# Optimization experiments

Measured on AMD Instinct MI355X. Metric: run time of the kernel, lower is better.

The kernel has to match this reference:

```python
import jax, jax.numpy as jnp
import numpy as np

WS = 8          # window_size
HEADS = 8
HEAD_DIM = 32
DIM = 256       # input_dim
DISP = WS // 2  # displacement for shifted windows
SCALE = HEAD_DIM ** -0.5
NEG = float('-inf')


def _create_mask(upper_lower, left_right):
    S = WS * WS
    m = np.zeros((S, S), np.float32)
    if upper_lower:
        m[-DISP * WS:, :-DISP * WS] = NEG
        m[:-DISP * WS, -DISP * WS:] = NEG
    if left_right:
        m = m.reshape(WS, WS, WS, WS)
        m[:, -DISP:, :, :-DISP] = NEG
        m[:, :-DISP, :, -DISP:] = NEG
        m = m.reshape(S, S)
    return m


def _shift_mask(nwh, nww):
    # per-window additive mask, [nW, S, S]
    S = WS * WS
    low = _create_mask(True, False)
    right = _create_mask(False, True)
    mask = np.zeros((nwh * nww, S, S), np.float32)
    mask[-nww:] += low                 # bottom row of windows
    mask[nww - 1::nww] += right        # rightmost column of windows
    return mask


def _rel_idx():
    coords = np.array([[x, y] for x in range(WS) for y in range(WS)])
    dist = coords[None, :, :] - coords[:, None, :] + (WS - 1)  # in [0, 2*WS-2]
    return dist[..., 0], dist[..., 1]


def setup_inputs() -> dict:
    key = jax.random.key(0)
    ks = jax.random.split(key, 5)
    B, H, W = 64, 64, 64
    inner = HEADS * HEAD_DIM
    return {
        "x": jax.random.normal(ks[0], (B, H, W, DIM), jnp.float32),
        "qkv_w": jax.random.normal(ks[1], (3 * inner, DIM), jnp.float32) * 0.02,
        "proj_w": jax.random.normal(ks[2], (DIM, inner), jnp.float32) * 0.02,
        "proj_b": jnp.zeros((DIM,), jnp.float32),
        "pos_emb": jax.random.normal(ks[3], (2 * WS - 1, 2 * WS - 1), jnp.float32),
    }


def reference(x, qkv_w, proj_w, proj_b, pos_emb):
    B, H, W, C = x.shape
    nwh, nww = H // WS, W // WS
    nW, S = nwh * nww, WS * WS

    x = jnp.roll(x, (-DISP, -DISP), axis=(1, 2))          # cyclic shift
    qkv = x @ qkv_w.T                                      # [B,H,W,3*inner]
    q, k, v = jnp.split(qkv, 3, axis=-1)

    def towin(t):  # [B,H,W,heads*d] -> [B,heads,nW,S,d]
        t = t.reshape(B, nwh, WS, nww, WS, HEADS, HEAD_DIM)
        return t.transpose(0, 5, 1, 3, 2, 4, 6).reshape(B, HEADS, nW, S, HEAD_DIM)

    q, k, v = towin(q), towin(k), towin(v)

    scores = jnp.einsum('bhwid,bhwjd->bhwij', q, k) * SCALE
    ri, ci = _rel_idx()
    scores = scores + pos_emb[ri, ci]                      # relative position bias [S,S]
    mask = jnp.asarray(_shift_mask(nwh, nww))              # [nW,S,S]
    scores = scores + mask[None, None]

    attn = jax.nn.softmax(scores, axis=-1)
    out = jnp.einsum('bhwij,bhwjd->bhwid', attn, v)        # [B,heads,nW,S,d]

    out = out.reshape(B, HEADS, nwh, nww, WS, WS, HEAD_DIM)
    out = out.transpose(0, 2, 4, 3, 5, 1, 6).reshape(B, H, W, HEADS * HEAD_DIM)

    out = out @ proj_w.T + proj_b
    out = jnp.roll(out, (DISP, DISP), axis=(1, 2))         # reverse cyclic shift
    return out
```

## Files before the change

kernel.cpp:

```cpp
#include <hip/hip_runtime.h>
#include <hip/hip_bf16.h>
#include <math.h>

typedef __bf16 bf16;
typedef bf16 bf16x8 __attribute__((ext_vector_type(8)));
typedef bf16 bf16x4 __attribute__((ext_vector_type(4)));
typedef float f32x4 __attribute__((ext_vector_type(4)));

#define MFMA16(A,B,C) __builtin_amdgcn_mfma_f32_16x16x32_bf16(A,B,C,0,0,0)

static constexpr int QKV_ELEMS  = 768 * 256;
static constexpr int PROJ_ELEMS = 256 * 256;

static __device__ __forceinline__ void lds_fence() {
    asm volatile("s_waitcnt lgkmcnt(0)" ::: "memory");
    __builtin_amdgcn_sched_barrier(0);
}

__global__ void cvt_weights(const float* __restrict__ qkv_w,
                            const float* __restrict__ proj_w,
                            bf16* __restrict__ wq, bf16* __restrict__ wp) {
    int i = blockIdx.x * 256 + threadIdx.x;
    if (i < QKV_ELEMS) wq[i] = (bf16)qkv_w[i];
    int j = i - QKV_ELEMS;
    if (j >= 0 && j < PROJ_ELEMS) wp[j] = (bf16)proj_w[j];
}

__global__ __launch_bounds__(512, 2)
void swin_fused(const float* __restrict__ x,
                const bf16* __restrict__ wqkv,
                const bf16* __restrict__ wproj,
                const float* __restrict__ proj_b,
                const float* __restrict__ pose_g,
                float* __restrict__ out)
{
    __shared__ alignas(16) unsigned char xbuf[64 * 512];
    __shared__ alignas(16) unsigned char wbuf[8][12288];
    __shared__ float pose[225];

    const int tid  = threadIdx.x;
    const int wave = tid >> 6, lane = tid & 63;
    const int hi   = lane >> 4, lo = lane & 15;
    const int b    = blockIdx.x >> 6;
    const int w    = blockIdx.x & 63;
    const int wh   = w >> 3, wwi = w & 7;
    const bool mlow = (wh == 7), mright = (wwi == 7);
    const f32x4 zero4 = {0.f, 0.f, 0.f, 0.f};

    if (tid < 225) pose[tid] = pose_g[tid];

    {
        int tok = tid >> 3, c0 = (tid & 7) * 32;
        int gy = ((wh << 3) + (tok >> 3) + 4) & 63;
        int gx = ((wwi << 3) + (tok & 7) + 4) & 63;
        const float* src = x + (((b << 6) + gy) * 64 + gx) * 256 + c0;
        #pragma unroll
        for (int cc = 0; cc < 4; ++cc) {
            float4 v0 = *(const float4*)(src + cc * 8);
            float4 v1 = *(const float4*)(src + cc * 8 + 4);
            bf16x8 bv;
            bv[0] = (bf16)v0.x; bv[1] = (bf16)v0.y; bv[2] = (bf16)v0.z; bv[3] = (bf16)v0.w;
            bv[4] = (bf16)v1.x; bv[5] = (bf16)v1.y; bv[6] = (bf16)v1.z; bv[7] = (bf16)v1.w;
            int chunk = ((c0 >> 3) + cc) ^ (tok & 7);
            *(bf16x8*)(xbuf + tok * 512 + (chunk << 4)) = bv;
        }
    }
    __syncthreads();

    unsigned char* qb = wbuf[wave];
    unsigned char* kb = qb + 4096;
    unsigned char* vb = qb + 8192;
    unsigned char* Pb = qb;
    const int h = wave;

    f32x4 acc[6][4];
    #pragma unroll
    for (int Mt = 0; Mt < 6; ++Mt)
        #pragma unroll
        for (int Nt = 0; Nt < 4; ++Nt) acc[Mt][Nt] = zero4;

    #pragma unroll
    for (int kk = 0; kk < 8; ++kk) {
        bf16x8 af[6], bx[4];
        #pragma unroll
        for (int Mt = 0; Mt < 6; ++Mt) {
            int wrow = (Mt >> 1) * 256 + h * 32 + ((Mt & 1) << 4) + lo;
            af[Mt] = *(const bf16x8*)(wqkv + wrow * 256 + kk * 32 + hi * 8);
        }
        #pragma unroll
        for (int Nt = 0; Nt < 4; ++Nt) {
            int tok = Nt * 16 + lo;
            bx[Nt] = *(const bf16x8*)(xbuf + tok * 512 + (((kk * 4 + hi) ^ (tok & 7)) << 4));
        }
        #pragma unroll
        for (int Mt = 0; Mt < 6; ++Mt)
            #pragma unroll
            for (int Nt = 0; Nt < 4; ++Nt)
                acc[Mt][Nt] = MFMA16(af[Mt], bx[Nt], acc[Mt][Nt]);
    }

    #pragma unroll
    for (int Mt = 0; Mt < 4; ++Mt) {
        unsigned char* base = (Mt < 2) ? qb : kb;
        int chunk_hi = ((Mt & 1) << 1) + (hi >> 1);
        #pragma unroll
        for (int Nt = 0; Nt < 4; ++Nt) {
            int tok = Nt * 16 + lo;
            bf16x4 v;
            #pragma unroll
            for (int r = 0; r < 4; ++r) v[r] = (bf16)acc[Mt][Nt][r];
            *(bf16x4*)(base + tok * 64 + ((chunk_hi ^ (tok & 3)) << 4) + ((hi & 1) << 3)) = v;
        }
    }
    #pragma unroll
    for (int Mt = 4; Mt < 6; ++Mt)
        #pragma unroll
        for (int Nt = 0; Nt < 4; ++Nt) {
            int tok = Nt * 16 + lo;
            #pragma unroll
            for (int r = 0; r < 4; ++r) {
                int d = ((Mt - 4) << 4) + 4 * hi + r;
                *(bf16*)(vb + d * 128 + (((tok >> 3) ^ (d & 7)) << 4) + ((tok & 7) << 1)) =
                    (bf16)acc[Mt][Nt][r];
            }
        }
    lds_fence();

    f32x4 sacc[4][4];
    {
        bf16x8 ka[4], qa[4];
        #pragma unroll
        for (int t = 0; t < 4; ++t) {
            int j = t * 16 + lo;
            ka[t] = *(const bf16x8*)(kb + j * 64 + ((hi ^ (j & 3)) << 4));
            qa[t] = *(const bf16x8*)(qb + j * 64 + ((hi ^ (j & 3)) << 4));
        }
        #pragma unroll
        for (int jt = 0; jt < 4; ++jt)
            #pragma unroll
            for (int it = 0; it < 4; ++it)
                sacc[jt][it] = MFMA16(ka[jt], qa[it], zero4);
    }

    float rinv[4];
    #pragma unroll
    for (int it = 0; it < 4; ++it) {
        float mx = -INFINITY;
        #pragma unroll
        for (int jt = 0; jt < 4; ++jt) {
            bool tilemask = mlow && ((it >= 2) != (jt >= 2));
            bool colmask  = mright && (((lo & 7) >= 4) != (hi & 1));
            #pragma unroll
            for (int r = 0; r < 4; ++r) {
                int drow = 2 * jt + (hi >> 1) - 2 * it - (lo >> 3) + 7;
                int dcol = 4 * (hi & 1) + r - (lo & 7) + 7;
                float s = sacc[jt][it][r] * 0.17677669529663687f + pose[drow * 15 + dcol];
                if (tilemask | colmask) s = -INFINITY;
                sacc[jt][it][r] = s;
                mx = fmaxf(mx, s);
            }
        }
        mx = fmaxf(mx, __shfl_xor(mx, 16));
        mx = fmaxf(mx, __shfl_xor(mx, 32));
        float sum = 0.f;
        #pragma unroll
        for (int jt = 0; jt < 4; ++jt)
            #pragma unroll
            for (int r = 0; r < 4; ++r) {
                float e = __expf(sacc[jt][it][r] - mx);
                sacc[jt][it][r] = e; sum += e;
            }
        sum += __shfl_xor(sum, 16);
        sum += __shfl_xor(sum, 32);
        rinv[it] = 1.0f / sum;
    }

    #pragma unroll
    for (int jt = 0; jt < 4; ++jt)
        #pragma unroll
        for (int it = 0; it < 4; ++it) {
            int i = it * 16 + lo;
            bf16x4 pv;
            #pragma unroll
            for (int r = 0; r < 4; ++r) pv[r] = (bf16)sacc[jt][it][r];
            int chunk = ((jt << 1) + (hi >> 1)) ^ (i & 7);
            *(bf16x4*)(Pb + i * 128 + (chunk << 4) + ((hi & 1) << 3)) = pv;
        }
    lds_fence();

    f32x4 oacc[2][4];
    #pragma unroll
    for (int dMt = 0; dMt < 2; ++dMt)
        #pragma unroll
        for (int it = 0; it < 4; ++it) oacc[dMt][it] = zero4;
    #pragma unroll
    for (int ks = 0; ks < 2; ++ks) {
        bf16x8 va[2], pr[4];
        #pragma unroll
        for (int dMt = 0; dMt < 2; ++dMt) {
            int d = dMt * 16 + lo;
            va[dMt] = *(const bf16x8*)(vb + d * 128 + (((ks * 4 + hi) ^ (d & 7)) << 4));
        }
        #pragma unroll
        for (int it = 0; it < 4; ++it) {
            int i = it * 16 + lo;
            pr[it] = *(const bf16x8*)(Pb + i * 128 + (((ks * 4 + hi) ^ (i & 7)) << 4));
        }
        #pragma unroll
        for (int dMt = 0; dMt < 2; ++dMt)
            #pragma unroll
            for (int it = 0; it < 4; ++it)
                oacc[dMt][it] = MFMA16(va[dMt], pr[it], oacc[dMt][it]);
    }

    __syncthreads();
    #pragma unroll
    for (int dMt = 0; dMt < 2; ++dMt)
        #pragma unroll
        for (int it = 0; it < 4; ++it) {
            int tok = it * 16 + lo;
            bf16x4 v;
            #pragma unroll
            for (int r = 0; r < 4; ++r) v[r] = (bf16)(oacc[dMt][it][r] * rinv[it]);
            int chunk = ((h << 2) + (dMt << 1) + (hi >> 1)) ^ (tok & 7);
            *(bf16x4*)(xbuf + tok * 512 + (chunk << 4) + ((hi & 1) << 3)) = v;
        }
    __syncthreads();

    f32x4 pacc[4][2];
    #pragma unroll
    for (int Mt = 0; Mt < 4; ++Mt)
        #pragma unroll
        for (int nt = 0; nt < 2; ++nt) pacc[Mt][nt] = zero4;
    #pragma unroll
    for (int kk = 0; kk < 8; ++kk) {
        bf16x8 aA[4], bB[2];
        #pragma unroll
        for (int Mt = 0; Mt < 4; ++Mt) {
            int tok = Mt * 16 + lo;
            aA[Mt] = *(const bf16x8*)(xbuf + tok * 512 + (((kk * 4 + hi) ^ (tok & 7)) << 4));
        }
        #pragma unroll
        for (int nt = 0; nt < 2; ++nt) {
            int c = wave * 32 + nt * 16 + lo;
            bB[nt] = *(const bf16x8*)(wproj + c * 256 + kk * 32 + hi * 8);
        }
        #pragma unroll
        for (int Mt = 0; Mt < 4; ++Mt)
            #pragma unroll
            for (int nt = 0; nt < 2; ++nt)
                pacc[Mt][nt] = MFMA16(aA[Mt], bB[nt], pacc[Mt][nt]);
    }
    #pragma unroll
    for (int nt = 0; nt < 2; ++nt) {
        int c = wave * 32 + nt * 16 + lo;
        float pb2 = proj_b[c];
        #pragma unroll
        for (int Mt = 0; Mt < 4; ++Mt)
            #pragma unroll
            for (int r = 0; r < 4; ++r) {
                int tok = Mt * 16 + 4 * hi + r;
                int fy = ((wh << 3) + (tok >> 3) + 4) & 63;
                int fx = ((wwi << 3) + (tok & 7) + 4) & 63;
                out[(((b << 6) + fy) * 64 + fx) * 256 + c] = pacc[Mt][nt][r] + pb2;
            }
    }
}

extern "C" void kernel_launch(void* const* d_in, const int* in_sizes, int n_in,
                              void* d_out, int out_size, void* d_ws, size_t ws_size,
                              hipStream_t stream) {
    const float* x       = (const float*)d_in[0];
    const float* qkv_w   = (const float*)d_in[1];
    const float* proj_w  = (const float*)d_in[2];
    const float* proj_b  = (const float*)d_in[3];
    const float* pos_emb = (const float*)d_in[4];

    bf16* wq = (bf16*)d_ws;
    bf16* wp = wq + QKV_ELEMS;

    cvt_weights<<<dim3((QKV_ELEMS + PROJ_ELEMS) / 256), dim3(256), 0, stream>>>(
        qkv_w, proj_w, wq, wp);
    swin_fused<<<dim3(64 * 64), dim3(512), 0, stream>>>(
        x, wq, wp, proj_b, pos_emb, (float*)d_out);
}
```

Baseline: 395.0 us.

## Keep Q/K/P in registers via lane shuffles, shrink LDS, raise occupancy

Q, K and the softmax probabilities are no longer staged through per-wave LDS buffers. Instead they are packed to bf16 pairs in registers and rearranged into MFMA operand fragments with cross-lane shuffles. The V projection is split into a separate MFMA pass, which cuts the per-wave LDS buffer from 12KB to 4KB, and launch bounds are raised from 2 to 4 blocks per CU. The x load is also rewritten into narrower float4 chunks. The aim is to reduce LDS traffic and footprint so more blocks fit per CU, at the cost of extra shuffle instructions and tighter register limits that may cause spills.

```diff
diff --git a/kernel.cpp b/kernel.cpp
--- a/kernel.cpp
+++ b/kernel.cpp
@@ -16,6 +16,29 @@
     asm volatile("s_waitcnt lgkmcnt(0)" ::: "memory");
     __builtin_amdgcn_sched_barrier(0);
 }
+
+static __device__ __forceinline__ unsigned pack2(float a, float b) {
+    bf16 xa = (bf16)a, xb = (bf16)b;
+    unsigned short ua, ub;
+    __builtin_memcpy(&ua, &xa, 2);
+    __builtin_memcpy(&ub, &xb, 2);
+    return (unsigned)ua | ((unsigned)ub << 16);
+}
+
+#define BUILD_FRAG(dst, PKL0, PKL1, PKH0, PKH1)                               \
+  {                                                                            \
+    int sA = ((lane & 16) << 1) + lo;                                          \
+    int sB = sA + 16;                                                          \
+    int a0 = __shfl((int)(PKL0), sA), a1 = __shfl((int)(PKL1), sA);            \
+    int a2 = __shfl((int)(PKL0), sB), a3 = __shfl((int)(PKL1), sB);            \
+    int b0 = __shfl((int)(PKH0), sA), b1 = __shfl((int)(PKH1), sA);            \
+    int b2 = __shfl((int)(PKH0), sB), b3 = __shfl((int)(PKH1), sB);            \
+    union { int w[4]; bf16x8 v; } u_;                                          \
+    bool uh_ = (lane >= 32);                                                   \
+    u_.w[0] = uh_ ? b0 : a0; u_.w[1] = uh_ ? b1 : a1;                          \
+    u_.w[2] = uh_ ? b2 : a2; u_.w[3] = uh_ ? b3 : a3;                          \
+    dst = u_.v;                                                                \
+  }
 
 __global__ void cvt_weights(const float* __restrict__ qkv_w,
                             const float* __restrict__ proj_w,
@@ -26,7 +49,7 @@
     if (j >= 0 && j < PROJ_ELEMS) wp[j] = (bf16)proj_w[j];
 }
 
-__global__ __launch_bounds__(512, 2)
+__global__ __launch_bounds__(512, 4)
 void swin_fused(const float* __restrict__ x,
                 const bf16* __restrict__ wqkv,
                 const bf16* __restrict__ wproj,
@@ -35,7 +58,7 @@
                 float* __restrict__ out)
 {
     __shared__ alignas(16) unsigned char xbuf[64 * 512];
-    __shared__ alignas(16) unsigned char wbuf[8][12288];
+    __shared__ alignas(16) unsigned char vbufs[8][4096];
     __shared__ float pose[225];
 
     const int tid  = threadIdx.x;
@@ -50,40 +73,35 @@
     if (tid < 225) pose[tid] = pose_g[tid];
 
     {
-        int tok = tid >> 3, c0 = (tid & 7) * 32;
+        int tok = tid >> 3, j = tid & 7;
         int gy = ((wh << 3) + (tok >> 3) + 4) & 63;
         int gx = ((wwi << 3) + (tok & 7) + 4) & 63;
-        const float* src = x + (((b << 6) + gy) * 64 + gx) * 256 + c0;
-        #pragma unroll
-        for (int cc = 0; cc < 4; ++cc) {
-            float4 v0 = *(const float4*)(src + cc * 8);
-            float4 v1 = *(const float4*)(src + cc * 8 + 4);
-            bf16x8 bv;
-            bv[0] = (bf16)v0.x; bv[1] = (bf16)v0.y; bv[2] = (bf16)v0.z; bv[3] = (bf16)v0.w;
-            bv[4] = (bf16)v1.x; bv[5] = (bf16)v1.y; bv[6] = (bf16)v1.z; bv[7] = (bf16)v1.w;
-            int chunk = ((c0 >> 3) + cc) ^ (tok & 7);
-            *(bf16x8*)(xbuf + tok * 512 + (chunk << 4)) = bv;
+        const float* src = x + (((b << 6) + gy) * 64 + gx) * 256;
+        #pragma unroll
+        for (int f = 0; f < 8; ++f) {
+            int c4 = f * 8 + j;
+            float4 v = *(const float4*)(src + c4 * 4);
+            bf16x4 bv;
+            bv[0] = (bf16)v.x; bv[1] = (bf16)v.y; bv[2] = (bf16)v.z; bv[3] = (bf16)v.w;
+            int chunk = (c4 >> 1) ^ (tok & 7);
+            *(bf16x4*)(xbuf + tok * 512 + (chunk << 4) + ((c4 & 1) << 3)) = bv;
         }
     }
     __syncthreads();
 
-    unsigned char* qb = wbuf[wave];
-    unsigned char* kb = qb + 4096;
-    unsigned char* vb = qb + 8192;
-    unsigned char* Pb = qb;
+    unsigned char* vb = vbufs[wave];
     const int h = wave;
 
-    f32x4 acc[6][4];
-    #pragma unroll
-    for (int Mt = 0; Mt < 6; ++Mt)
+    f32x4 acc[4][4];
+    #pragma unroll
+    for (int Mt = 0; Mt < 4; ++Mt)
         #pragma unroll
         for (int Nt = 0; Nt < 4; ++Nt) acc[Mt][Nt] = zero4;
-
     #pragma unroll
     for (int kk = 0; kk < 8; ++kk) {
-        bf16x8 af[6], bx[4];
-        #pragma unroll
-        for (int Mt = 0; Mt < 6; ++Mt) {
+        bf16x8 af[4], bx[4];
+        #pragma unroll
+        for (int Mt = 0; Mt < 4; ++Mt) {
             int wrow = (Mt >> 1) * 256 + h * 32 + ((Mt & 1) << 4) + lo;
             af[Mt] = *(const bf16x8*)(wqkv + wrow * 256 + kk * 32 + hi * 8);
         }
@@ -93,70 +111,88 @@
             bx[Nt] = *(const bf16x8*)(xbuf + tok * 512 + (((kk * 4 + hi) ^ (tok & 7)) << 4));
         }
         #pragma unroll
-        for (int Mt = 0; Mt < 6; ++Mt)
+        for (int Mt = 0; Mt < 4; ++Mt)
             #pragma unroll
             for (int Nt = 0; Nt < 4; ++Nt)
                 acc[Mt][Nt] = MFMA16(af[Mt], bx[Nt], acc[Mt][Nt]);
     }
-
-    #pragma unroll
-    for (int Mt = 0; Mt < 4; ++Mt) {
-        unsigned char* base = (Mt < 2) ? qb : kb;
-        int chunk_hi = ((Mt & 1) << 1) + (hi >> 1);
-        #pragma unroll
-        for (int Nt = 0; Nt < 4; ++Nt) {
-            int tok = Nt * 16 + lo;
-            bf16x4 v;
-            #pragma unroll
-            for (int r = 0; r < 4; ++r) v[r] = (bf16)acc[Mt][Nt][r];
-            *(bf16x4*)(base + tok * 64 + ((chunk_hi ^ (tok & 3)) << 4) + ((hi & 1) << 3)) = v;
-        }
-    }
-    #pragma unroll
-    for (int Mt = 4; Mt < 6; ++Mt)
-        #pragma unroll
-        for (int Nt = 0; Nt < 4; ++Nt) {
-            int tok = Nt * 16 + lo;
-            #pragma unroll
-            for (int r = 0; r < 4; ++r) {
-                int d = ((Mt - 4) << 4) + 4 * hi + r;
-                *(bf16*)(vb + d * 128 + (((tok >> 3) ^ (d & 7)) << 4) + ((tok & 7) << 1)) =
-                    (bf16)acc[Mt][Nt][r];
-            }
-        }
-    lds_fence();
-
-    f32x4 sacc[4][4];
+    unsigned pkQ[2][4][2], pkK[2][4][2];
+    #pragma unroll
+    for (int Mt = 0; Mt < 2; ++Mt)
+        #pragma unroll
+        for (int Nt = 0; Nt < 4; ++Nt)
+            #pragma unroll
+            for (int p = 0; p < 2; ++p) {
+                pkQ[Mt][Nt][p] = pack2(acc[Mt][Nt][2 * p],     acc[Mt][Nt][2 * p + 1]);
+                pkK[Mt][Nt][p] = pack2(acc[2 + Mt][Nt][2 * p], acc[2 + Mt][Nt][2 * p + 1]);
+            }
+
     {
-        bf16x8 ka[4], qa[4];
-        #pragma unroll
-        for (int t = 0; t < 4; ++t) {
-            int j = t * 16 + lo;
-            ka[t] = *(const bf16x8*)(kb + j * 64 + ((hi ^ (j & 3)) << 4));
-            qa[t] = *(const bf16x8*)(qb + j * 64 + ((hi ^ (j & 3)) << 4));
-        }
-        #pragma unroll
-        for (int jt = 0; jt < 4; ++jt)
-            #pragma unroll
-            for (int it = 0; it < 4; ++it)
-                sacc[jt][it] = MFMA16(ka[jt], qa[it], zero4);
-    }
-
+        f32x4 accv[2][4];
+        #pragma unroll
+        for (int vm = 0; vm < 2; ++vm)
+            #pragma unroll
+            for (int Nt = 0; Nt < 4; ++Nt) accv[vm][Nt] = zero4;
+        #pragma unroll
+        for (int kk = 0; kk < 8; ++kk) {
+            bf16x8 af[2], bx[4];
+            #pragma unroll
+            for (int vm = 0; vm < 2; ++vm) {
+                int wrow = 512 + h * 32 + (vm << 4) + lo;
+                af[vm] = *(const bf16x8*)(wqkv + wrow * 256 + kk * 32 + hi * 8);
+            }
+            #pragma unroll
+            for (int Nt = 0; Nt < 4; ++Nt) {
+                int tok = Nt * 16 + lo;
+                bx[Nt] = *(const bf16x8*)(xbuf + tok * 512 + (((kk * 4 + hi) ^ (tok & 7)) << 4));
+            }
+            #pragma unroll
+            for (int vm = 0; vm < 2; ++vm)
+                #pragma unroll
+                for (int Nt = 0; Nt < 4; ++Nt)
+                    accv[vm][Nt] = MFMA16(af[vm], bx[Nt], accv[vm][Nt]);
+        }
+        #pragma unroll
+        for (int vm = 0; vm < 2; ++vm)
+            #pragma unroll
+            for (int Nt = 0; Nt < 4; ++Nt) {
+                int tok = Nt * 16 + lo;
+                #pragma unroll
+                for (int r = 0; r < 4; ++r) {
+                    int d = (vm << 4) + 4 * hi + r;
+                    *(bf16*)(vb + d * 128 + (((tok >> 3) ^ (d & 7)) << 4) + ((tok & 7) << 1)) =
+                        (bf16)accv[vm][Nt][r];
+                }
+            }
+    }
+
+    bf16x8 kA[4];
+    #pragma unroll
+    for (int jt = 0; jt < 4; ++jt)
+        BUILD_FRAG(kA[jt], pkK[0][jt][0], pkK[0][jt][1], pkK[1][jt][0], pkK[1][jt][1]);
+
+    unsigned pkP[4][4][2];
     float rinv[4];
+    const bool colmask_ = mright && (((lo & 7) >= 4) != (hi & 1));
     #pragma unroll
     for (int it = 0; it < 4; ++it) {
+        bf16x8 qB;
+        BUILD_FRAG(qB, pkQ[0][it][0], pkQ[0][it][1], pkQ[1][it][0], pkQ[1][it][1]);
+        f32x4 s4[4];
+        #pragma unroll
+        for (int jt = 0; jt < 4; ++jt) s4[jt] = MFMA16(kA[jt], qB, zero4);
+
         float mx = -INFINITY;
         #pragma unroll
         for (int jt = 0; jt < 4; ++jt) {
             bool tilemask = mlow && ((it >= 2) != (jt >= 2));
-            bool colmask  = mright && (((lo & 7) >= 4) != (hi & 1));
             #pragma unroll
             for (int r = 0; r < 4; ++r) {
                 int drow = 2 * jt + (hi >> 1) - 2 * it - (lo >> 3) + 7;
                 int dcol = 4 * (hi & 1) + r - (lo & 7) + 7;
-                float s = sacc[jt][it][r] * 0.17677669529663687f + pose[drow * 15 + dcol];
-                if (tilemask | colmask) s = -INFINITY;
-                sacc[jt][it][r] = s;
+                float s = s4[jt][r] * 0.17677669529663687f + pose[drow * 15 + dcol];
+                if (tilemask | colmask_) s = -INFINITY;
+                s4[jt][r] = s;
                 mx = fmaxf(mx, s);
             }
         }
@@ -167,35 +203,28 @@
         for (int jt = 0; jt < 4; ++jt)
             #pragma unroll
             for (int r = 0; r < 4; ++r) {
-                float e = __expf(sacc[jt][it][r] - mx);
-                sacc[jt][it][r] = e; sum += e;
+                float e = __expf(s4[jt][r] - mx);
+                s4[jt][r] = e; sum += e;
             }
         sum += __shfl_xor(sum, 16);
         sum += __shfl_xor(sum, 32);
         rinv[it] = 1.0f / sum;
-    }
-
-    #pragma unroll
-    for (int jt = 0; jt < 4; ++jt)
-        #pragma unroll
-        for (int it = 0; it < 4; ++it) {
-            int i = it * 16 + lo;
-            bf16x4 pv;
-            #pragma unroll
-            for (int r = 0; r < 4; ++r) pv[r] = (bf16)sacc[jt][it][r];
-            int chunk = ((jt << 1) + (hi >> 1)) ^ (i & 7);
-            *(bf16x4*)(Pb + i * 128 + (chunk << 4) + ((hi & 1) << 3)) = pv;
-        }
+        #pragma unroll
+        for (int jt = 0; jt < 4; ++jt)
+            #pragma unroll
+            for (int p = 0; p < 2; ++p)
+                pkP[jt][it][p] = pack2(s4[jt][2 * p], s4[jt][2 * p + 1]);
+    }
+
+    f32x4 oacc[2][4];
+    #pragma unroll
+    for (int dMt = 0; dMt < 2; ++dMt)
+        #pragma unroll
+        for (int it = 0; it < 4; ++it) oacc[dMt][it] = zero4;
     lds_fence();
-
-    f32x4 oacc[2][4];
-    #pragma unroll
-    for (int dMt = 0; dMt < 2; ++dMt)
-        #pragma unroll
-        for (int it = 0; it < 4; ++it) oacc[dMt][it] = zero4;
     #pragma unroll
     for (int ks = 0; ks < 2; ++ks) {
-        bf16x8 va[2], pr[4];
+        bf16x8 va[2];
         #pragma unroll
         for (int dMt = 0; dMt < 2; ++dMt) {
             int d = dMt * 16 + lo;
@@ -203,14 +232,13 @@
         }
         #pragma unroll
         for (int it = 0; it < 4; ++it) {
-            int i = it * 16 + lo;
-            pr[it] = *(const bf16x8*)(Pb + i * 128 + (((ks * 4 + hi) ^ (i & 7)) << 4));
-        }
-        #pragma unroll
-        for (int dMt = 0; dMt < 2; ++dMt)
-            #pragma unroll
-            for (int it = 0; it < 4; ++it)
-                oacc[dMt][it] = MFMA16(va[dMt], pr[it], oacc[dMt][it]);
+            bf16x8 pB;
+            BUILD_FRAG(pB, pkP[2 * ks][it][0], pkP[2 * ks][it][1],
+                           pkP[2 * ks + 1][it][0], pkP[2 * ks + 1][it][1]);
+            #pragma unroll
+            for (int dMt = 0; dMt < 2; ++dMt)
+                oacc[dMt][it] = MFMA16(va[dMt], pB, oacc[dMt][it]);
+        }
     }
 
     __syncthreads();
```

New measurement: 730.9 us. 1.85x slower.
